# Optimization experiments

Hardware: AMD Instinct MI355X
Metric: run time of the kernel (lower is better)

## Reference

```python
import jax, jax.numpy as jnp
import numpy as np

H = 256          # hidden_dim
D = 64           # dim_dynamic
R = 49           # pooler_resolution ** 2
N = 2000         # bs * num_proposals
EPS = 1e-5


def _ln(x, g, b):
    m = jnp.mean(x, axis=-1, keepdims=True)
    v = jnp.mean(jnp.square(x - m), axis=-1, keepdims=True)
    return (x - m) * jax.lax.rsqrt(v + EPS) * g + b


def setup_inputs() -> dict:
    key = jax.random.key(0)
    ks = jax.random.split(key, 6)
    pro_features = jax.random.normal(ks[0], (1, N, H), dtype=jnp.float32)
    roi_features = jax.random.normal(ks[1], (R, N, H), dtype=jnp.float32)
    # dynamic_layer: Linear(H, num_dynamic * H * D) with num_dynamic = 2
    W_dyn = jax.random.normal(ks[2], (H, 2 * H * D), dtype=jnp.float32) * 0.02
    b_dyn = jnp.zeros((2 * H * D,), dtype=jnp.float32)
    # out_layer: Linear(H * R, H)
    W_out = jax.random.normal(ks[3], (H * R, H), dtype=jnp.float32) * 0.02
    b_out = jnp.zeros((H,), dtype=jnp.float32)
    g1 = jnp.ones((D,), dtype=jnp.float32); b1 = jnp.zeros((D,), dtype=jnp.float32)
    g2 = jnp.ones((H,), dtype=jnp.float32); b2 = jnp.zeros((H,), dtype=jnp.float32)
    g3 = jnp.ones((H,), dtype=jnp.float32); b3 = jnp.zeros((H,), dtype=jnp.float32)
    return {"pro_features": pro_features, "roi_features": roi_features,
            "W_dyn": W_dyn, "b_dyn": b_dyn, "W_out": W_out, "b_out": b_out,
            "g1": g1, "b1": b1, "g2": g2, "b2": b2, "g3": g3, "b3": b3}


def reference(pro_features, roi_features, W_dyn, b_dyn, W_out, b_out,
              g1, b1, g2, b2, g3, b3):
    # roi_features: (R, N, H) -> features: (N, R, H)
    feats = jnp.transpose(roi_features, (1, 0, 2))
    # per-instance dynamic parameters: (N, 2*H*D)
    params = pro_features[0] @ W_dyn + b_dyn
    num_params = H * D
    p1 = params[:, :num_params].reshape(-1, H, D)   # (N, H, D)
    p2 = params[:, num_params:].reshape(-1, D, H)   # (N, D, H)
    f = jnp.einsum('nrh,nhd->nrd', feats, p1)       # bmm 1
    f = jax.nn.relu(_ln(f, g1, b1))
    f = jnp.einsum('nrd,ndh->nrh', f, p2)           # bmm 2
    f = jax.nn.relu(_ln(f, g2, b2))
    f = f.reshape(f.shape[0], R * H)                # flatten(1)
    f = jax.nn.relu(_ln(f @ W_out + b_out, g3, b3))
    return f  # (N, H)
```

## Files before the change

kernel.cpp:

```cpp
#include <hip/hip_runtime.h>

typedef unsigned short u16;
typedef __attribute__((ext_vector_type(8))) short short8;
typedef __attribute__((ext_vector_type(4))) float f32x4;

#define N_INST 2000
#define H_DIM 256
#define D_DIM 64
#define R_DIM 49
#define LN_EPS 1e-5f
#define SPLITK 14

__device__ __forceinline__ u16 f2bf(float f) {
  union { float f; unsigned int i; } x; x.f = f;
  unsigned int r = x.i + 0x7fffu + ((x.i >> 16) & 1u);
  return (u16)(r >> 16);
}
__device__ __forceinline__ float bf2f(u16 u) {
  union { unsigned int i; float f; } x; x.i = ((unsigned int)u) << 16; return x.f;
}
__device__ __forceinline__ short8 ld8(const u16* p) {
  return *reinterpret_cast<const short8*>(p);
}
__device__ __forceinline__ short8 pack8(float4 a, float4 b) {
  short8 r;
  r[0] = (short)f2bf(a.x); r[1] = (short)f2bf(a.y);
  r[2] = (short)f2bf(a.z); r[3] = (short)f2bf(a.w);
  r[4] = (short)f2bf(b.x); r[5] = (short)f2bf(b.y);
  r[6] = (short)f2bf(b.z); r[7] = (short)f2bf(b.w);
  return r;
}
__device__ __forceinline__ f32x4 mfma16(short8 a, short8 b, f32x4 c) {
  return __builtin_amdgcn_mfma_f32_16x16x32_bf16(a, b, c, 0, 0, 0);
}
__device__ __forceinline__ void wave_reduce2(float& s, float& s2) {
#pragma unroll
  for (int off = 32; off > 0; off >>= 1) {
    s  += __shfl_down(s, off);
    s2 += __shfl_down(s2, off);
  }
  s = __shfl(s, 0); s2 = __shfl(s2, 0);
}
__device__ __forceinline__ void gload16(const u16* g, u16* l) {
  __builtin_amdgcn_global_load_lds(
      (const __attribute__((address_space(1))) void*)g,
      (__attribute__((address_space(3))) void*)l, 16, 0, 0);
}

__global__ __launch_bounds__(256) void cast_pro(const float* __restrict__ in,
                                                u16* __restrict__ out, int n4) {
  for (int i = blockIdx.x * 256 + threadIdx.x; i < n4; i += gridDim.x * 256) {
    float4 v = ((const float4*)in)[i];
    u16* op = out + i * 4;
    op[0] = f2bf(v.x); op[1] = f2bf(v.y); op[2] = f2bf(v.z); op[3] = f2bf(v.w);
  }
}

__global__ __launch_bounds__(256) void cast_wdyn(const float* __restrict__ W,
                                                 u16* __restrict__ WT, int half) {
  __shared__ u16 T[64][65];
  const int tid = threadIdx.x;
  const int wave = tid >> 6, lane = tid & 63;
  const int b = blockIdx.x;
  const int kt = b >> 8;
  long colbase, rowbase; int rstride;
  if (half == 0) {
    int h = b & 255;
    colbase = (long)h * 64; rowbase = h; rstride = 256;
  } else {
    int d = b & 63, hc = (b >> 6) & 3;
    colbase = 16384L + d * 256 + hc * 64;
    rowbase = 16384L + hc * 4096 + d; rstride = 64;
  }
#pragma unroll
  for (int i = 0; i < 16; ++i) {
    int kk = wave * 16 + i;
    int k = kt * 64 + kk;
    T[kk][lane] = f2bf(W[(long)k * 32768 + colbase + lane]);
  }
  __syncthreads();
#pragma unroll
  for (int i = 0; i < 16; ++i) {
    int jj = wave * 16 + i;
    long ro = rowbase + (long)jj * rstride;
    WT[ro * 256 + kt * 64 + lane] = T[lane][jj];
  }
}

__global__ __launch_bounds__(256) void cast_wout(const float* __restrict__ W,
                                                 u16* __restrict__ WT) {
  __shared__ u16 T[64][65];
  const int tid = threadIdx.x;
  const int wave = tid >> 6, lane = tid & 63;
  const int kt = blockIdx.x >> 2, ct = blockIdx.x & 3;
#pragma unroll
  for (int i = 0; i < 16; ++i) {
    int kk = wave * 16 + i;
    long k = (long)kt * 64 + kk;
    T[kk][lane] = f2bf(W[k * 256 + ct * 64 + lane]);
  }
  __syncthreads();
#pragma unroll
  for (int i = 0; i < 16; ++i) {
    int cc = wave * 16 + i;
    long c = (long)ct * 64 + cc;
    WT[c * 12544 + (long)kt * 64 + lane] = T[lane][cc];
  }
}

__global__ __launch_bounds__(256, 3) void gemm128(
    const u16* __restrict__ A, int lda, int M,
    const u16* __restrict__ BT, int ldbt,
    const float* __restrict__ bias, int bias_mode,
    void* __restrict__ Cout, int ldc, long c_stride_s,
    int ksteps, int n_blocks, int out_f32)
{
  union Smem {
    struct { u16 a[2][128 * 32]; u16 b[2][128 * 32]; } s;
    u16 cb[128 * 128];
  };
  __shared__ Smem sm;

  const int tid = threadIdx.x;
  const int wave = tid >> 6, lane = tid & 63;
  const int quad = lane >> 4, l16 = lane & 15;
  const int wm = wave >> 1, wn = wave & 1;
  const int bid = blockIdx.x;
  const int mblk = bid / n_blocks, nblk = bid - mblk * n_blocks;
  const int m0 = mblk * 128, n0 = nblk * 128;
  const int s = blockIdx.y;
  const int kb = s * ksteps * 32;

  const int cl = tid & 3;
  const int r0 = tid >> 2, r1 = 64 + (tid >> 2);
  const int cg0 = cl ^ ((r0 >> 1) & 3);
  const int cg1 = cl ^ ((r1 >> 1) & 3);
  int ga0 = m0 + r0; if (ga0 >= M) ga0 = M - 1;
  int ga1 = m0 + r1; if (ga1 >= M) ga1 = M - 1;
  const u16* gA0 = A + (long)ga0 * lda + kb + cg0 * 8;
  const u16* gA1 = A + (long)ga1 * lda + kb + cg1 * 8;
  const u16* gB0 = BT + (long)(n0 + r0) * ldbt + kb + cg0 * 8;
  const u16* gB1 = BT + (long)(n0 + r1) * ldbt + kb + cg1 * 8;

  int fAoff[4], fBoff[4];
#pragma unroll
  for (int i = 0; i < 4; ++i) {
    int rt = wm * 64 + i * 16 + l16;
    fAoff[i] = rt * 32 + (quad ^ ((rt >> 1) & 3)) * 8;
    int ct = wn * 64 + i * 16 + l16;
    fBoff[i] = ct * 32 + (quad ^ ((ct >> 1) & 3)) * 8;
  }

  f32x4 acc[4][4];
#pragma unroll
  for (int mi = 0; mi < 4; ++mi)
#pragma unroll
    for (int ni = 0; ni < 4; ++ni) acc[mi][ni] = f32x4{0.f, 0.f, 0.f, 0.f};

  gload16(gA0, &sm.s.a[0][tid * 8]);
  gload16(gA1, &sm.s.a[0][(tid + 256) * 8]);
  gload16(gB0, &sm.s.b[0][tid * 8]);
  gload16(gB1, &sm.s.b[0][(tid + 256) * 8]);

  for (int ks = 0; ks < ksteps; ++ks) {
    const int cur = ks & 1, nxt = cur ^ 1;
    __syncthreads();
    if (ks + 1 < ksteps) {
      const int ko = (ks + 1) * 32;
      gload16(gA0 + ko, &sm.s.a[nxt][tid * 8]);
      gload16(gA1 + ko, &sm.s.a[nxt][(tid + 256) * 8]);
      gload16(gB0 + ko, &sm.s.b[nxt][tid * 8]);
      gload16(gB1 + ko, &sm.s.b[nxt][(tid + 256) * 8]);
    }
    short8 av[4], bv[4];
#pragma unroll
    for (int i = 0; i < 4; ++i) {
      av[i] = ld8(&sm.s.a[cur][fAoff[i]]);
      bv[i] = ld8(&sm.s.b[cur][fBoff[i]]);
    }
#pragma unroll
    for (int mi = 0; mi < 4; ++mi)
#pragma unroll
      for (int ni = 0; ni < 4; ++ni)
        acc[mi][ni] = mfma16(av[mi], bv[ni], acc[mi][ni]);
  }

  if (!out_f32) {
    float bvv[4];
#pragma unroll
    for (int ni = 0; ni < 4; ++ni) {
      int col = n0 + wn * 64 + ni * 16 + l16;
      int bi = col;
      if (bias_mode == 3)
        bi = (col < 16384) ? (((col & 255) << 6) + (col >> 8))
                           : (16384 + ((col & 63) << 8) + ((col >> 6) & 255));
      bvv[ni] = bias ? bias[bi] : 0.f;
    }
    __syncthreads();
#pragma unroll
    for (int mi = 0; mi < 4; ++mi)
#pragma unroll
      for (int ni = 0; ni < 4; ++ni)
#pragma unroll
        for (int i = 0; i < 4; ++i) {
          int row = wm * 64 + mi * 16 + quad * 4 + i;
          int col = wn * 64 + ni * 16 + l16;
          sm.cb[row * 128 + col] = f2bf(acc[mi][ni][i] + bvv[ni]);
        }
    __syncthreads();
    u16* Cp = (u16*)Cout;
#pragma unroll
    for (int j = 0; j < 8; ++j) {
      int lin = j * 2048 + tid * 8;
      int row = lin >> 7, col = lin & 127;
      int grow = m0 + row;
      if (grow < M)
        *reinterpret_cast<short8*>(Cp + (long)grow * ldc + n0 + col) =
            ld8(&sm.cb[lin]);
    }
  } else {
    float* Cp = (float*)Cout + (long)s * c_stride_s;
#pragma unroll
    for (int mi = 0; mi < 4; ++mi)
#pragma unroll
      for (int ni = 0; ni < 4; ++ni) {
        int col = n0 + wn * 64 + ni * 16 + l16;
#pragma unroll
        for (int i = 0; i < 4; ++i) {
          int row = m0 + wm * 64 + mi * 16 + quad * 4 + i;
          if (row < M) Cp[(long)row * ldc + col] = acc[mi][ni][i];
        }
      }
  }
}

__global__ __launch_bounds__(256, 2) void bmm12_ln(
    const float* __restrict__ roi,
    const u16* __restrict__ P12,
    const float* __restrict__ g1, const float* __restrict__ b1,
    const float* __restrict__ g2, const float* __restrict__ b2,
    u16* __restrict__ f2n)
{
  __shared__ u16 p1b[16384];
  __shared__ u16 p2b[16384];
  __shared__ u16 f1b[4096];
  const int n = blockIdx.x;
  const int tid = threadIdx.x;
  const int wave = tid >> 6, lane = tid & 63;
  const int quad = lane >> 4, l16 = lane & 15;
  const int wstripe = wave * 16;

  const u16* P1n = P12 + (long)n * 32768;
#pragma unroll
  for (int j = 0; j < 8; ++j) {
    int lc = j * 256 + tid;
    int d = lc >> 5, c = lc & 31;
    int cg = (c & 24) | ((c & 7) ^ (d & 7));
    gload16(P1n + d * 256 + cg * 8, &p1b[lc * 8]);
  }
  const u16* P2n = P12 + (long)n * 32768 + 16384;
#pragma unroll
  for (int j = 0; j < 8; ++j) {
    int lc = j * 256 + tid;
    int h = lc >> 3, c = lc & 7;
    gload16(P2n + h * 64 + (c ^ (h & 7)) * 8, &p2b[lc * 8]);
  }
  int r = wstripe + l16;
  int rr = (r < R_DIM) ? r : 0;
  const float* Arow = roi + ((long)rr * N_INST + n) * H_DIM + quad * 8;
  float4 rv[16];
#pragma unroll
  for (int ks = 0; ks < 8; ++ks) {
    rv[2 * ks]     = ((const float4*)(Arow + ks * 32))[0];
    rv[2 * ks + 1] = ((const float4*)(Arow + ks * 32))[1];
  }
  float gv1[4], bv1[4];
#pragma unroll
  for (int sub = 0; sub < 4; ++sub) {
    gv1[sub] = g1[sub * 16 + l16]; bv1[sub] = b1[sub * 16 + l16];
  }
  __syncthreads();

  short8 sa[8];
#pragma unroll
  for (int ks = 0; ks < 8; ++ks) sa[ks] = pack8(rv[2 * ks], rv[2 * ks + 1]);

  f32x4 acc1[4];
#pragma unroll
  for (int i = 0; i < 4; ++i) acc1[i] = f32x4{0.f, 0.f, 0.f, 0.f};
#pragma unroll
  for (int ks = 0; ks < 8; ++ks) {
#pragma unroll
    for (int sub = 0; sub < 4; ++sub) {
      int d = sub * 16 + l16;
      int q = ks * 4 + quad;
      int c = (q & 24) | ((q & 7) ^ (d & 7));
      acc1[sub] = mfma16(sa[ks], ld8(&p1b[d * 256 + c * 8]), acc1[sub]);
    }
  }

  {
    float s1[4], s2[4];
#pragma unroll
    for (int i = 0; i < 4; ++i) {
      s1[i] = 0.f; s2[i] = 0.f;
#pragma unroll
      for (int sub = 0; sub < 4; ++sub) {
        float v = acc1[sub][i]; s1[i] += v; s2[i] += v * v;
      }
    }
#pragma unroll
    for (int m = 1; m < 16; m <<= 1)
#pragma unroll
      for (int i = 0; i < 4; ++i) {
        s1[i] += __shfl_xor(s1[i], m, 16);
        s2[i] += __shfl_xor(s2[i], m, 16);
      }
#pragma unroll
    for (int i = 0; i < 4; ++i) {
      float mean = s1[i] * (1.f / 64.f);
      float var = s2[i] * (1.f / 64.f) - mean * mean;
      float rs = rsqrtf(var + LN_EPS);
      int row = wstripe + quad * 4 + i;
#pragma unroll
      for (int sub = 0; sub < 4; ++sub) {
        float y = fmaxf((acc1[sub][i] - mean) * rs * gv1[sub] + bv1[sub], 0.f);
        int kc = (sub * 2 + (l16 >> 3)) ^ (row & 7);
        f1b[row * 64 + kc * 8 + (l16 & 7)] = f2bf(y);
      }
    }
  }

  short8 af2[2];
#pragma unroll
  for (int ks = 0; ks < 2; ++ks) {
    int row = wstripe + l16;
    int c2 = (ks * 4 + quad) ^ (row & 7);
    af2[ks] = ld8(&f1b[row * 64 + c2 * 8]);
  }
  f32x4 acc2[16];
#pragma unroll
  for (int i = 0; i < 16; ++i) acc2[i] = f32x4{0.f, 0.f, 0.f, 0.f};
#pragma unroll
  for (int ks = 0; ks < 2; ++ks) {
#pragma unroll
    for (int sub = 0; sub < 16; ++sub) {
      int h = sub * 16 + l16;
      int c = (ks * 4 + quad) ^ (h & 7);
      acc2[sub] = mfma16(af2[ks], ld8(&p2b[h * 64 + c * 8]), acc2[sub]);
    }
  }

  float mean2[4], rs2[4];
  {
    float s1[4], s2[4];
#pragma unroll
    for (int i = 0; i < 4; ++i) {
      s1[i] = 0.f; s2[i] = 0.f;
#pragma unroll
      for (int sub = 0; sub < 16; ++sub) {
        float v = acc2[sub][i]; s1[i] += v; s2[i] += v * v;
      }
    }
#pragma unroll
    for (int m = 1; m < 16; m <<= 1)
#pragma unroll
      for (int i = 0; i < 4; ++i) {
        s1[i] += __shfl_xor(s1[i], m, 16);
        s2[i] += __shfl_xor(s2[i], m, 16);
      }
#pragma unroll
    for (int i = 0; i < 4; ++i) {
      mean2[i] = s1[i] * (1.f / 256.f);
      float var = s2[i] * (1.f / 256.f) - mean2[i] * mean2[i];
      rs2[i] = rsqrtf(var + LN_EPS);
    }
  }
  __syncthreads();

#pragma unroll
  for (int i = 0; i < 4; ++i) {
    int row = wstripe + quad * 4 + i;
    if (row < R_DIM) {
#pragma unroll
      for (int sub = 0; sub < 16; ++sub)
        p1b[row * 264 + sub * 16 + l16] =
            f2bf((acc2[sub][i] - mean2[i]) * rs2[i]);
    }
  }
  __syncthreads();

  u16* f2out = f2n + (long)n * (R_DIM * H_DIM);
  for (int t = tid; t < R_DIM * 32; t += 256) {
    int row = t >> 5, c = t & 31;
    short8 z8 = ld8(&p1b[row * 264 + c * 8]);
    const float4* gp = (const float4*)(g2 + c * 8);
    const float4* bp = (const float4*)(b2 + c * 8);
    float4 ga = gp[0], gb = gp[1], ba = bp[0], bb = bp[1];
    short8 y;
    y[0] = (short)f2bf(fmaxf(bf2f((u16)z8[0]) * ga.x + ba.x, 0.f));
    y[1] = (short)f2bf(fmaxf(bf2f((u16)z8[1]) * ga.y + ba.y, 0.f));
    y[2] = (short)f2bf(fmaxf(bf2f((u16)z8[2]) * ga.z + ba.z, 0.f));
    y[3] = (short)f2bf(fmaxf(bf2f((u16)z8[3]) * ga.w + ba.w, 0.f));
    y[4] = (short)f2bf(fmaxf(bf2f((u16)z8[4]) * gb.x + bb.x, 0.f));
    y[5] = (short)f2bf(fmaxf(bf2f((u16)z8[5]) * gb.y + bb.y, 0.f));
    y[6] = (short)f2bf(fmaxf(bf2f((u16)z8[6]) * gb.z + bb.z, 0.f));
    y[7] = (short)f2bf(fmaxf(bf2f((u16)z8[7]) * gb.w + bb.w, 0.f));
    *reinterpret_cast<short8*>(f2out + row * 256 + c * 8) = y;
  }
}

__global__ __launch_bounds__(64) void ln3_k(
    const float* __restrict__ partial,
    const float* __restrict__ b_out,
    const float* __restrict__ g3, const float* __restrict__ b3,
    float* __restrict__ out)
{
  const int n = blockIdx.x;
  const int lane = threadIdx.x;
  float x[4], sv = 0.f, s2 = 0.f;
#pragma unroll
  for (int j = 0; j < 4; ++j) {
    int h = lane + 64 * j;
    float v = b_out[h];
#pragma unroll
    for (int ss = 0; ss < SPLITK; ++ss)
      v += partial[((long)ss * N_INST + n) * H_DIM + h];
    x[j] = v; sv += v; s2 += v * v;
  }
  wave_reduce2(sv, s2);
  float mean = sv * (1.f / 256.f);
  float var = s2 * (1.f / 256.f) - mean * mean;
  float rs = rsqrtf(var + LN_EPS);
#pragma unroll
  for (int j = 0; j < 4; ++j) {
    int h = lane + 64 * j;
    float y = fmaxf((x[j] - mean) * rs * g3[h] + b3[h], 0.f);
    out[(long)n * H_DIM + h] = y;
  }
}

extern "C" void kernel_launch(void* const* d_in, const int* in_sizes, int n_in,
                              void* d_out, int out_size, void* d_ws, size_t ws_size,
                              hipStream_t stream) {
  const float* pro  = (const float*)d_in[0];
  const float* roi  = (const float*)d_in[1];
  const float* Wdyn = (const float*)d_in[2];
  const float* bdyn = (const float*)d_in[3];
  const float* Wout = (const float*)d_in[4];
  const float* bout = (const float*)d_in[5];
  const float* g1 = (const float*)d_in[6];
  const float* b1 = (const float*)d_in[7];
  const float* g2 = (const float*)d_in[8];
  const float* b2 = (const float*)d_in[9];
  const float* g3 = (const float*)d_in[10];
  const float* b3 = (const float*)d_in[11];
  float* out = (float*)d_out;

  char* ws = (char*)d_ws;
  u16* proB  = (u16*)ws;
  u16* WdynT = (u16*)(ws + 1024000);
  u16* WoutT = (u16*)(ws + 17801216);
  u16* P12   = (u16*)(ws + 24223744);
  u16* f2n   = (u16*)(ws + 155295744);
  float* partial = (float*)(ws + 24223744);

  dim3 blk(256);

  cast_pro<<<dim3(500), blk, 0, stream>>>(pro, proB, 512000 / 4);
  cast_wdyn<<<dim3(1024), blk, 0, stream>>>(Wdyn, WdynT, 0);
  cast_wdyn<<<dim3(1024), blk, 0, stream>>>(Wdyn, WdynT, 1);
  cast_wout<<<dim3(784), blk, 0, stream>>>(Wout, WoutT);

  gemm128<<<dim3(16 * 256, 1), blk, 0, stream>>>(
      proB, H_DIM, N_INST, WdynT, H_DIM, bdyn, 3,
      (void*)P12, 32768, 0L, 8, 256, 0);
  bmm12_ln<<<dim3(N_INST), blk, 0, stream>>>(roi, P12, g1, b1, g2, b2, f2n);
  gemm128<<<dim3(16 * 2, SPLITK), blk, 0, stream>>>(
      f2n, R_DIM * H_DIM, N_INST, WoutT, R_DIM * H_DIM, nullptr, 0,
      (void*)partial, H_DIM, (long)N_INST * H_DIM, 28, 2, 1);
  ln3_k<<<dim3(N_INST), dim3(64), 0, stream>>>(partial, bout, g3, b3, out);
}
```

Baseline: 330.7 us.

## Split bmm2 across waves by H columns, drop p2 LDS buffer, merge cast launches

The second per-instance matmul is restructured. Each wave now owns a 64-column slice of H across all rows, and its p2 fragments are loaded straight from global memory into registers, so the 32KB p2 shared buffer is no longer needed. With less LDS per block, launch bounds are raised to allow 4 blocks per CU. Because each wave now holds only part of every row, LayerNorm-2 statistics are combined across waves through a small LDS scratch area plus an extra barrier. The two cast_wdyn launches are also merged into one grid to save a launch.

```diff
diff --git a/kernel.cpp b/kernel.cpp
--- a/kernel.cpp
+++ b/kernel.cpp
@@ -57,11 +57,12 @@
 }
 
 __global__ __launch_bounds__(256) void cast_wdyn(const float* __restrict__ W,
-                                                 u16* __restrict__ WT, int half) {
+                                                 u16* __restrict__ WT) {
   __shared__ u16 T[64][65];
   const int tid = threadIdx.x;
   const int wave = tid >> 6, lane = tid & 63;
-  const int b = blockIdx.x;
+  const int half = blockIdx.x >> 10;
+  const int b = blockIdx.x & 1023;
   const int kt = b >> 8;
   long colbase, rowbase; int rstride;
   if (half == 0) {
@@ -234,16 +235,15 @@
   }
 }
 
-__global__ __launch_bounds__(256, 2) void bmm12_ln(
+__global__ __launch_bounds__(256, 4) void bmm12_ln(
     const float* __restrict__ roi,
     const u16* __restrict__ P12,
     const float* __restrict__ g1, const float* __restrict__ b1,
     const float* __restrict__ g2, const float* __restrict__ b2,
     u16* __restrict__ f2n)
 {
-  __shared__ u16 p1b[16384];
-  __shared__ u16 p2b[16384];
-  __shared__ u16 f1b[4096];
+  __shared__ __align__(16) u16 p1b[16384];
+  __shared__ __align__(16) u16 f1b[4096];
   const int n = blockIdx.x;
   const int tid = threadIdx.x;
   const int wave = tid >> 6, lane = tid & 63;
@@ -258,32 +258,31 @@
     int cg = (c & 24) | ((c & 7) ^ (d & 7));
     gload16(P1n + d * 256 + cg * 8, &p1b[lc * 8]);
   }
-  const u16* P2n = P12 + (long)n * 32768 + 16384;
-#pragma unroll
-  for (int j = 0; j < 8; ++j) {
-    int lc = j * 256 + tid;
-    int h = lc >> 3, c = lc & 7;
-    gload16(P2n + h * 64 + (c ^ (h & 7)) * 8, &p2b[lc * 8]);
-  }
   int r = wstripe + l16;
   int rr = (r < R_DIM) ? r : 0;
   const float* Arow = roi + ((long)rr * N_INST + n) * H_DIM + quad * 8;
-  float4 rv[16];
+  short8 sa[8];
 #pragma unroll
   for (int ks = 0; ks < 8; ++ks) {
-    rv[2 * ks]     = ((const float4*)(Arow + ks * 32))[0];
-    rv[2 * ks + 1] = ((const float4*)(Arow + ks * 32))[1];
-  }
+    float4 va = ((const float4*)(Arow + ks * 32))[0];
+    float4 vb = ((const float4*)(Arow + ks * 32))[1];
+    sa[ks] = pack8(va, vb);
+  }
+  const u16* P2n = P12 + (long)n * 32768 + 16384;
+  short8 pf[4][2];
+#pragma unroll
+  for (int hs = 0; hs < 4; ++hs)
+#pragma unroll
+    for (int ks = 0; ks < 2; ++ks) {
+      int h = wave * 64 + hs * 16 + l16;
+      pf[hs][ks] = ld8(P2n + h * 64 + (ks * 4 + quad) * 8);
+    }
   float gv1[4], bv1[4];
 #pragma unroll
   for (int sub = 0; sub < 4; ++sub) {
     gv1[sub] = g1[sub * 16 + l16]; bv1[sub] = b1[sub * 16 + l16];
   }
   __syncthreads();
-
-  short8 sa[8];
-#pragma unroll
-  for (int ks = 0; ks < 8; ++ks) sa[ks] = pack8(rv[2 * ks], rv[2 * ks + 1]);
 
   f32x4 acc1[4];
 #pragma unroll
@@ -330,64 +329,78 @@
       }
     }
   }
-
-  short8 af2[2];
+  __syncthreads();
+
+  f32x4 acc2[4][4];
+#pragma unroll
+  for (int rs = 0; rs < 4; ++rs)
+#pragma unroll
+    for (int hs = 0; hs < 4; ++hs) acc2[rs][hs] = f32x4{0.f, 0.f, 0.f, 0.f};
 #pragma unroll
   for (int ks = 0; ks < 2; ++ks) {
-    int row = wstripe + l16;
-    int c2 = (ks * 4 + quad) ^ (row & 7);
-    af2[ks] = ld8(&f1b[row * 64 + c2 * 8]);
-  }
-  f32x4 acc2[16];
-#pragma unroll
-  for (int i = 0; i < 16; ++i) acc2[i] = f32x4{0.f, 0.f, 0.f, 0.f};
-#pragma unroll
-  for (int ks = 0; ks < 2; ++ks) {
-#pragma unroll
-    for (int sub = 0; sub < 16; ++sub) {
-      int h = sub * 16 + l16;
-      int c = (ks * 4 + quad) ^ (h & 7);
-      acc2[sub] = mfma16(af2[ks], ld8(&p2b[h * 64 + c * 8]), acc2[sub]);
-    }
-  }
-
-  float mean2[4], rs2[4];
-  {
-    float s1[4], s2[4];
+#pragma unroll
+    for (int rs = 0; rs < 4; ++rs) {
+      int row = rs * 16 + l16;
+      int c2 = (ks * 4 + quad) ^ (row & 7);
+      short8 af = ld8(&f1b[row * 64 + c2 * 8]);
+#pragma unroll
+      for (int hs = 0; hs < 4; ++hs)
+        acc2[rs][hs] = mfma16(af, pf[hs][ks], acc2[rs][hs]);
+    }
+  }
+
+  float s1[4][4], s2[4][4];
+#pragma unroll
+  for (int rs = 0; rs < 4; ++rs)
 #pragma unroll
     for (int i = 0; i < 4; ++i) {
-      s1[i] = 0.f; s2[i] = 0.f;
-#pragma unroll
-      for (int sub = 0; sub < 16; ++sub) {
-        float v = acc2[sub][i]; s1[i] += v; s2[i] += v * v;
-      }
-    }
-#pragma unroll
-    for (int m = 1; m < 16; m <<= 1)
+      float a = 0.f, b = 0.f;
+#pragma unroll
+      for (int hs = 0; hs < 4; ++hs) {
+        float v = acc2[rs][hs][i]; a += v; b += v * v;
+      }
+      s1[rs][i] = a; s2[rs][i] = b;
+    }
+#pragma unroll
+  for (int m = 1; m < 16; m <<= 1)
+#pragma unroll
+    for (int rs = 0; rs < 4; ++rs)
 #pragma unroll
       for (int i = 0; i < 4; ++i) {
-        s1[i] += __shfl_xor(s1[i], m, 16);
-        s2[i] += __shfl_xor(s2[i], m, 16);
-      }
+        s1[rs][i] += __shfl_xor(s1[rs][i], m, 16);
+        s2[rs][i] += __shfl_xor(s2[rs][i], m, 16);
+      }
+  float2* lnst = reinterpret_cast<float2*>(&p1b[14336]);
+  if (l16 == 0) {
+#pragma unroll
+    for (int rs = 0; rs < 4; ++rs)
+#pragma unroll
+      for (int i = 0; i < 4; ++i) {
+        int row = rs * 16 + quad * 4 + i;
+        lnst[row * 4 + wave] = float2{s1[rs][i], s2[rs][i]};
+      }
+  }
+  __syncthreads();
+
+#pragma unroll
+  for (int rs = 0; rs < 4; ++rs)
 #pragma unroll
     for (int i = 0; i < 4; ++i) {
-      mean2[i] = s1[i] * (1.f / 256.f);
-      float var = s2[i] * (1.f / 256.f) - mean2[i] * mean2[i];
-      rs2[i] = rsqrtf(var + LN_EPS);
-    }
-  }
-  __syncthreads();
-
-#pragma unroll
-  for (int i = 0; i < 4; ++i) {
-    int row = wstripe + quad * 4 + i;
-    if (row < R_DIM) {
-#pragma unroll
-      for (int sub = 0; sub < 16; ++sub)
-        p1b[row * 264 + sub * 16 + l16] =
-            f2bf((acc2[sub][i] - mean2[i]) * rs2[i]);
-    }
-  }
+      int row = rs * 16 + quad * 4 + i;
+      f32x4 qa = *reinterpret_cast<const f32x4*>(&lnst[row * 4]);
+      f32x4 qb = *reinterpret_cast<const f32x4*>(&lnst[row * 4 + 2]);
+      float S1 = qa[0] + qa[2] + qb[0] + qb[2];
+      float S2 = qa[1] + qa[3] + qb[1] + qb[3];
+      float mean = S1 * (1.f / 256.f);
+      float var = S2 * (1.f / 256.f) - mean * mean;
+      float rsq = rsqrtf(var + LN_EPS);
+      if (row < R_DIM) {
+#pragma unroll
+        for (int hs = 0; hs < 4; ++hs)
+          p1b[row * 264 + wave * 64 + hs * 16 + l16] =
+              f2bf((acc2[rs][hs][i] - mean) * rsq);
+      }
+    }
   __syncthreads();
 
   u16* f2out = f2n + (long)n * (R_DIM * H_DIM);
@@ -468,8 +481,7 @@
   dim3 blk(256);
 
   cast_pro<<<dim3(500), blk, 0, stream>>>(pro, proB, 512000 / 4);
-  cast_wdyn<<<dim3(1024), blk, 0, stream>>>(Wdyn, WdynT, 0);
-  cast_wdyn<<<dim3(1024), blk, 0, stream>>>(Wdyn, WdynT, 1);
+  cast_wdyn<<<dim3(2048), blk, 0, stream>>>(Wdyn, WdynT);
   cast_wout<<<dim3(784), blk, 0, stream>>>(Wout, WoutT);
 
   gemm128<<<dim3(16 * 256, 1), blk, 0, stream>>>(
```

Measured after the change: 326.4 us. No clear change (-1.3%).
